# Performance work log

Measured on AMD Instinct MI355X. Metric: run time of the kernel, lower is better.

## Reference

```python
import jax, jax.numpy as jnp
import numpy as np

B = 1024      # batch
DF = 2048     # dim_feat (hard-coded in module)
DIM = 128     # contrastive feature dim
C = 8192      # class_num
P = 8         # pos_size_per_cls
N = 4         # neg_size_per_cls
BN_EPS = 1e-5


def _l2norm(x, axis):
    n = jnp.sqrt(jnp.sum(x * x, axis=axis, keepdims=True))
    return x / jnp.maximum(n, 1e-12)


def setup_inputs() -> dict:
    key = jax.random.key(0)
    ks = jax.random.split(key, 12)
    inp = {
        'mid_feat_q': jax.random.normal(ks[0], (B, DF), jnp.float32),
        'mid_feat_k': jax.random.normal(ks[1], (B, DF), jnp.float32),
        'labels_q': jax.random.randint(ks[2], (B,), 0, C, jnp.int32),
        'labels_k': jax.random.randint(ks[3], (B,), 0, C, jnp.int32),
        'W1': jax.random.normal(ks[4], (DF, DF), jnp.float32) * 0.02,
        'b1': jnp.zeros((DF,), jnp.float32),
        'gamma': jnp.ones((DF,), jnp.float32),
        'beta': jnp.zeros((DF,), jnp.float32),
        'W2': jax.random.normal(ks[5], (DF, DIM), jnp.float32) * 0.02,
        'b2': jnp.zeros((DIM,), jnp.float32),
        'Wlin': jax.random.normal(ks[6], (DF, C), jnp.float32) * 0.02,
        'blin': jnp.zeros((C,), jnp.float32),
        'neg_queue': _l2norm(jax.random.normal(ks[7], (DIM, N * C), jnp.float32), axis=0),
        'pos_queue': _l2norm(jax.random.normal(ks[8], (DIM, P * C), jnp.float32), axis=0),
        'neg_ptr': jnp.zeros((C,), jnp.int32),
        'pos_ptr': jnp.zeros((C,), jnp.int32),
    }
    return inp


def _mlp(x, W1, b1, gamma, beta, W2, b2):
    # Linear -> BatchNorm1d (training: batch stats, biased var) -> ReLU -> Linear
    h = x @ W1 + b1
    mu = jnp.mean(h, axis=0)
    var = jnp.var(h, axis=0)
    h = (h - mu) * jax.lax.rsqrt(var + BN_EPS) * gamma + beta
    h = jax.nn.relu(h)
    return h @ W2 + b2


def reference(mid_feat_q, mid_feat_k, labels_q, labels_k,
              W1, b1, gamma, beta, W2, b2, Wlin, blin,
              neg_queue, pos_queue, neg_ptr, pos_ptr):
    feat_q = _l2norm(_mlp(mid_feat_q, W1, b1, gamma, beta, W2, b2), axis=1)
    feat_k = _l2norm(_mlp(mid_feat_k, W1, b1, gamma, beta, W2, b2), axis=1)

    # per-sample positive block gather: pos_queue[:, l*P:(l+1)*P]
    posq = pos_queue.reshape(DIM, C, P)          # (dim, C, P)
    pg = posq[:, labels_q, :]                    # (dim, B, P)
    pos_list = jnp.einsum('bd,dbp->bp', feat_q, pg)   # (B, P)

    # negatives: full sim then drop each sample's own-class block of N columns
    full_neg = feat_q @ neg_queue                # (B, N*C)
    cols = jnp.arange(N * (C - 1), dtype=jnp.int32)
    idx = cols[None, :] + N * (cols[None, :] >= labels_q[:, None] * N).astype(jnp.int32)
    neg_list = jnp.take_along_axis(full_neg, idx, axis=1)  # (B, N*(C-1))

    sim_batch = feat_q @ feat_k.T                # (B, B)
    labels_batch = (labels_q[:, None] == labels_k[None, :]).astype(jnp.float32)

    sim_con = jnp.concatenate([sim_batch, pos_list, neg_list], axis=1)
    labels_con = jnp.concatenate(
        [labels_batch, jnp.ones_like(pos_list), jnp.zeros_like(neg_list)], axis=1)

    logit_cls_q = mid_feat_q @ Wlin + blin
    logit_cls_k = mid_feat_k @ Wlin + blin

    # sequential dequeue/enqueue over the key batch (world_size=1 all_gather)
    def step(carry, inp):
        nq, nptr, pq, pptr = carry
        kv, c = inp
        npos = nptr[c]
        nq = nq.at[:, c * N + npos].set(kv)
        nptr = nptr.at[c].set((npos + 1) % N)
        ppos = pptr[c]
        pq = pq.at[:, c * P + ppos].set(kv)
        pptr = pptr.at[c].set((ppos + 1) % P)
        return (nq, nptr, pq, pptr), None

    (neg_queue2, neg_ptr2, pos_queue2, pos_ptr2), _ = jax.lax.scan(
        step, (neg_queue, neg_ptr, pos_queue, pos_ptr),
        (jax.lax.stop_gradient(feat_k), labels_k))

    return (sim_con, labels_con, logit_cls_q, logit_cls_k,
            neg_queue2, pos_queue2, neg_ptr2, pos_ptr2)
```

## Files before the change

kernel.cpp:

```cpp
#include <hip/hip_runtime.h>

typedef unsigned short u16;
typedef __bf16 bf16x8 __attribute__((ext_vector_type(8)));
typedef unsigned short ushort8 __attribute__((ext_vector_type(8)));
typedef float f32x4 __attribute__((ext_vector_type(4)));

typedef const __attribute__((address_space(1))) void gv_t;
typedef __attribute__((address_space(3))) void lv_t;

__device__ __forceinline__ u16 f2bf(float f) {
    union { float f; unsigned u; } x; x.f = f;
    unsigned r = x.u + 0x7fffu + ((x.u >> 16) & 1u);
    return (u16)(r >> 16);
}
__device__ __forceinline__ float bf2f(u16 h) {
    union { unsigned u; float f; } x; x.u = ((unsigned)h) << 16; return x.f;
}
__device__ __forceinline__ bf16x8 as_bf(ushort8 u) {
    union { ushort8 u; bf16x8 b; } x; x.u = u; return x.b;
}

__global__ void k_cast(const float* __restrict__ in, u16* __restrict__ out, long nvec) {
    long i = (long)blockIdx.x * blockDim.x + threadIdx.x;
    long stride = (long)gridDim.x * blockDim.x;
    for (; i < nvec; i += stride) {
        float4 v = ((const float4*)in)[i];
        u16 o[4] = {f2bf(v.x), f2bf(v.y), f2bf(v.z), f2bf(v.w)};
        *(unsigned long long*)(out + i * 4) = *(unsigned long long*)o;
    }
}

__global__ void k_castT(const float* __restrict__ in, u16* __restrict__ out,
                        int R, int C) {
    __shared__ u16 tile[32][33];
    int c0 = blockIdx.x * 32, r0 = blockIdx.y * 32;
    int tx = threadIdx.x, ty = threadIdx.y;
#pragma unroll
    for (int i = 0; i < 4; i++)
        tile[ty + 8 * i][tx] = f2bf(in[(size_t)(r0 + ty + 8 * i) * C + c0 + tx]);
    __syncthreads();
#pragma unroll
    for (int i = 0; i < 4; i++)
        out[(size_t)(c0 + ty + 8 * i) * R + r0 + tx] = tile[tx][ty + 8 * i];
}

template <int EPI>
__global__ __launch_bounds__(256, 2) void gemm_bt(
    const u16* A0, const u16* A1, const u16* __restrict__ Bt,
    const float* __restrict__ bias, u16* H0, u16* H1, float* C0, float* C1,
    int lda, int ldb, long long ldc, int n_tiles, int Kchunk,
    const int* __restrict__ labels) {
    __shared__ u16 Al[128 * 32];
    __shared__ u16 Bl[128 * 32];
    const int bx = blockIdx.x;
    const int by = blockIdx.y % n_tiles;
    const int kc = blockIdx.y / n_tiles;
    const int half = blockIdx.z;
    const u16* A = half ? A1 : A0;
    const int m0 = bx * 128, n0 = by * 128;
    const int t = threadIdx.x;
    const int w = t >> 6, l = t & 63;
    const int wm = (w & 1) * 64, wn = (w >> 1) * 64;
    const int quad = l >> 4, ln = l & 15;
    const int srow = t >> 2;
    const int sk = (t & 3) * 8;

    f32x4 acc[4][4];
#pragma unroll
    for (int i = 0; i < 4; i++)
#pragma unroll
        for (int j = 0; j < 4; j++) acc[i][j] = f32x4{};

    u16* lAw = Al + (w << 4) * 32;
    u16* lBw = Bl + (w << 4) * 32;

    const int k_begin = kc * Kchunk;
    for (int k0 = k_begin; k0 < k_begin + Kchunk; k0 += 32) {
        if (k0 != k_begin) __syncthreads();
#pragma unroll
        for (int i = 0; i < 2; i++) {
            __builtin_amdgcn_global_load_lds(
                (gv_t*)(A + (size_t)(m0 + srow + i * 64) * lda + k0 + sk),
                (lv_t*)(lAw + i * 64 * 32), 16, 0, 0);
            __builtin_amdgcn_global_load_lds(
                (gv_t*)(Bt + (size_t)(n0 + srow + i * 64) * ldb + k0 + sk),
                (lv_t*)(lBw + i * 64 * 32), 16, 0, 0);
        }
        __syncthreads();
        bf16x8 af[4], bb[4];
#pragma unroll
        for (int i = 0; i < 4; i++) {
            af[i] = as_bf(*(const ushort8*)(Al + (wm + i * 16 + ln) * 32 + quad * 8));
            bb[i] = as_bf(*(const ushort8*)(Bl + (wn + i * 16 + ln) * 32 + quad * 8));
        }
#pragma unroll
        for (int i = 0; i < 4; i++)
#pragma unroll
            for (int j = 0; j < 4; j++)
                acc[i][j] = __builtin_amdgcn_mfma_f32_16x16x32_bf16(af[i], bb[j], acc[i][j], 0, 0, 0);
    }

    u16* Hs = half ? H1 : H0;
    float* Cs = half ? C1 : C0;
#pragma unroll
    for (int i = 0; i < 4; i++) {
        int row = m0 + wm + i * 16 + quad * 4;
#pragma unroll
        for (int j = 0; j < 4; j++) {
            int col = n0 + wn + j * 16 + ln;
            float bv = 0.f;
            if (EPI == 0 || EPI == 3) { if (bias) bv = bias[col]; }
#pragma unroll
            for (int r = 0; r < 4; r++) {
                int rr = row + r;
                float v = acc[i][j][r] + bv;
                if (EPI == 0) {
                    Cs[(size_t)rr * ldc + col] = v;
                } else if (EPI == 3) {
                    Hs[(size_t)rr * ldc + col] = f2bf(v);
                } else if (EPI == 2) {
                    atomicAdd(Cs + (size_t)rr * ldc + col, v);
                } else {
                    int L4 = labels[rr] * 4;
                    if (col < L4)
                        Cs[(size_t)rr * ldc + 1032 + col] = v;
                    else if (col >= L4 + 4)
                        Cs[(size_t)rr * ldc + 1032 + col - 4] = v;
                }
            }
        }
    }
}

__global__ void k_bn_stats(const u16* __restrict__ Hq, const u16* __restrict__ Hk,
                           float* __restrict__ ps, float* __restrict__ ps2) {
    int half = blockIdx.z;
    const u16* H = half ? Hk : Hq;
    int col = blockIdx.x * 256 + threadIdx.x;
    int r0 = blockIdx.y * 64;
    float s = 0.f, s2 = 0.f;
    for (int r = 0; r < 64; r++) {
        float v = bf2f(H[(size_t)(r0 + r) * 2048 + col]);
        s += v; s2 += v * v;
    }
    size_t o = ((size_t)half * 16 + blockIdx.y) * 2048 + col;
    ps[o] = s; ps2[o] = s2;
}

__global__ void k_bn_final(const float* __restrict__ ps, const float* __restrict__ ps2,
                           const float* __restrict__ gamma, const float* __restrict__ beta,
                           float* __restrict__ scale, float* __restrict__ shift) {
    int idx = blockIdx.x * 256 + threadIdx.x;
    int half = idx >> 11, col = idx & 2047;
    float s = 0.f, s2 = 0.f;
    for (int rb = 0; rb < 16; rb++) {
        size_t o = ((size_t)half * 16 + rb) * 2048 + col;
        s += ps[o]; s2 += ps2[o];
    }
    float mu = s * (1.f / 1024.f);
    float var = s2 * (1.f / 1024.f) - mu * mu;
    float sc = gamma[col] * rsqrtf(var + 1e-5f);
    shift[half * 2048 + col] = beta[col] - mu * sc;
    scale[half * 2048 + col] = sc;
}

__global__ void k_bn_apply(u16* Hq, u16* Hk, const float* __restrict__ scale,
                           const float* __restrict__ shift) {
    int row = blockIdx.x, half = blockIdx.y;
    u16* H = half ? Hk : Hq;
    int col = threadIdx.x * 8;
    ushort8 h = *(ushort8*)(H + (size_t)row * 2048 + col);
    ushort8 o;
#pragma unroll
    for (int k = 0; k < 8; k++) {
        float v = bf2f(h[k]) * scale[half * 2048 + col + k] + shift[half * 2048 + col + k];
        o[k] = f2bf(fmaxf(v, 0.f));
    }
    *(ushort8*)(H + (size_t)row * 2048 + col) = o;
}

__global__ void k_l2norm(const float* __restrict__ Fq, const float* __restrict__ Fk,
                         const float* __restrict__ b2, float* fqf, float* fkf,
                         u16* fqh, u16* fkh) {
    int row = blockIdx.x, half = blockIdx.y, d = threadIdx.x;
    const float* F = half ? Fk : Fq;
    float x = F[(size_t)row * 128 + d] + b2[d];
    float ss = x * x;
#pragma unroll
    for (int off = 32; off >= 1; off >>= 1) ss += __shfl_down(ss, off);
    __shared__ float p[2];
    if ((threadIdx.x & 63) == 0) p[threadIdx.x >> 6] = ss;
    __syncthreads();
    float n = sqrtf(p[0] + p[1]);
    float v = x / fmaxf(n, 1e-12f);
    (half ? fkf : fqf)[(size_t)row * 128 + d] = v;
    (half ? fkh : fqh)[(size_t)row * 128 + d] = f2bf(v);
}

__global__ void k_poslist(const float* __restrict__ fqf, const float* __restrict__ pq,
                          const int* __restrict__ lq, float* out0) {
    int b = blockIdx.x, lane = threadIdx.x;
    int base = lq[b] * 8;
    float acc[8] = {0, 0, 0, 0, 0, 0, 0, 0};
    for (int d = lane; d < 128; d += 64) {
        float f = fqf[(size_t)b * 128 + d];
        const float* pp = pq + (size_t)d * 65536 + base;
        float4 v0 = *(const float4*)pp;
        float4 v1 = *(const float4*)(pp + 4);
        acc[0] += f * v0.x; acc[1] += f * v0.y; acc[2] += f * v0.z; acc[3] += f * v0.w;
        acc[4] += f * v1.x; acc[5] += f * v1.y; acc[6] += f * v1.z; acc[7] += f * v1.w;
    }
#pragma unroll
    for (int off = 32; off >= 1; off >>= 1)
#pragma unroll
        for (int p = 0; p < 8; p++) acc[p] += __shfl_down(acc[p], off);
    if (lane == 0) {
#pragma unroll
        for (int p = 0; p < 8; p++)
            out0[(size_t)b * 33796 + 1024 + p] = acc[p];
    }
}

__global__ void k_labels(const int* __restrict__ lq, const int* __restrict__ lk,
                         float* __restrict__ out1) {
    int b = blockIdx.y;
    int j0 = (blockIdx.x * 256 + threadIdx.x) * 8;
    if (j0 >= 33796) return;
    float* o = out1 + (size_t)b * 33796;
    if (j0 >= 1032 && j0 + 8 <= 33796) {
        float4 z = {0.f, 0.f, 0.f, 0.f};
        *(float4*)(o + j0) = z;
        *(float4*)(o + j0 + 4) = z;
    } else {
        int Lq = lq[b];
        for (int k = 0; k < 8 && j0 + k < 33796; k++) {
            int j = j0 + k;
            o[j] = (j < 1024) ? ((Lq == lk[j]) ? 1.f : 0.f) : (j < 1032 ? 1.f : 0.f);
        }
    }
}

__global__ void k_copyf4(const float* __restrict__ src, float* __restrict__ dst, long nvec) {
    long i = (long)blockIdx.x * blockDim.x + threadIdx.x;
    long stride = (long)gridDim.x * blockDim.x;
    for (; i < nvec; i += stride) ((float4*)dst)[i] = ((const float4*)src)[i];
}

__global__ void k_rank(const int* __restrict__ lk, const int* __restrict__ nptr,
                       const int* __restrict__ pptr, int* __restrict__ counts,
                       int* __restrict__ colN, int* __restrict__ colP) {
    __shared__ int lab[1024];
    int b = threadIdx.x;
    lab[b] = lk[b];
    __syncthreads();
    int c = lab[b];
    int rank = 0, count = 0;
    for (int i = 0; i < 1024; i++) {
        int m = (lab[i] == c);
        count += m;
        rank += (i < b) ? m : 0;
    }
    if (rank == count - 1) counts[c] = count;
    colN[b] = (rank >= count - 4) ? c * 4 + (nptr[c] + rank) % 4 : -1;
    colP[b] = (rank >= count - 8) ? c * 8 + (pptr[c] + rank) % 8 : -1;
}

__global__ void k_scatter(const float* __restrict__ fkf, const int* __restrict__ colN,
                          const int* __restrict__ colP, float* outN, float* outP) {
    int b = blockIdx.x, d = threadIdx.x;
    float v = fkf[(size_t)b * 128 + d];
    int cn = colN[b];
    if (cn >= 0) outN[(size_t)d * 32768 + cn] = v;
    int cp = colP[b];
    if (cp >= 0) outP[(size_t)d * 65536 + cp] = v;
}

__global__ void k_ptrs(const int* __restrict__ nptr, const int* __restrict__ pptr,
                       const int* __restrict__ counts, float* outN, float* outP) {
    int c = blockIdx.x * 256 + threadIdx.x;
    int cnt = counts[c];
    outN[c] = (float)((nptr[c] + cnt) & 3);
    outP[c] = (float)((pptr[c] + cnt) & 7);
}

extern "C" void kernel_launch(void* const* d_in, const int* in_sizes, int n_in,
                              void* d_out, int out_size, void* d_ws, size_t ws_size,
                              hipStream_t stream) {
    const float* midq = (const float*)d_in[0];
    const float* midk = (const float*)d_in[1];
    const int* lq     = (const int*)d_in[2];
    const int* lk     = (const int*)d_in[3];
    const float* W1   = (const float*)d_in[4];
    const float* b1   = (const float*)d_in[5];
    const float* gamma= (const float*)d_in[6];
    const float* beta = (const float*)d_in[7];
    const float* W2   = (const float*)d_in[8];
    const float* b2   = (const float*)d_in[9];
    const float* Wlin = (const float*)d_in[10];
    const float* blin = (const float*)d_in[11];
    const float* nq   = (const float*)d_in[12];
    const float* pq   = (const float*)d_in[13];
    const int* nptr   = (const int*)d_in[14];
    const int* pptr   = (const int*)d_in[15];
    (void)in_sizes; (void)n_in; (void)out_size; (void)ws_size;

    float* out = (float*)d_out;
    const size_t O0 = 0;
    const size_t O1 = 34607104;
    const size_t O2 = 69214208;
    const size_t O3 = 77602816;
    const size_t O4 = 85991424;
    const size_t O5 = 90185728;
    const size_t O6 = 98574336;
    const size_t O7 = 98582528;

    char* ws = (char*)d_ws;
    size_t off = 0;
    auto alloc = [&](size_t bytes) -> char* {
        char* p = ws + off;
        off = (off + bytes + 255) & ~(size_t)255;
        return p;
    };
    u16* W1t   = (u16*)alloc((size_t)2048 * 2048 * 2);
    u16* WlinT = (u16*)alloc((size_t)8192 * 2048 * 2);
    u16* W2t   = (u16*)alloc((size_t)128 * 2048 * 2);
    u16* nqT   = (u16*)alloc((size_t)32768 * 128 * 2);
    u16* midqh = (u16*)alloc((size_t)1024 * 2048 * 2);
    u16* midkh = (u16*)alloc((size_t)1024 * 2048 * 2);
    u16* Hq    = (u16*)alloc((size_t)1024 * 2048 * 2);
    u16* Hk    = (u16*)alloc((size_t)1024 * 2048 * 2);
    float* Fq  = (float*)alloc((size_t)1024 * 128 * 4);
    float* Fk  = (float*)alloc((size_t)1024 * 128 * 4);
    float* fqf = (float*)alloc((size_t)1024 * 128 * 4);
    float* fkf = (float*)alloc((size_t)1024 * 128 * 4);
    u16* fqh   = (u16*)alloc((size_t)1024 * 128 * 2);
    u16* fkh   = (u16*)alloc((size_t)1024 * 128 * 2);
    float* ps  = (float*)alloc((size_t)2 * 16 * 2048 * 4);
    float* ps2 = (float*)alloc((size_t)2 * 16 * 2048 * 4);
    float* scaleA = (float*)alloc((size_t)2 * 2048 * 4);
    float* shiftA = (float*)alloc((size_t)2 * 2048 * 4);
    int* counts = (int*)alloc(8192 * 4);
    int* colN   = (int*)alloc(1024 * 4);
    int* colP   = (int*)alloc(1024 * 4);

    k_cast<<<1024, 256, 0, stream>>>(midq, midqh, (long)1024 * 2048 / 4);
    k_cast<<<1024, 256, 0, stream>>>(midk, midkh, (long)1024 * 2048 / 4);
    dim3 tb(32, 8);
    k_castT<<<dim3(64, 64), tb, 0, stream>>>(W1, W1t, 2048, 2048);
    k_castT<<<dim3(256, 64), tb, 0, stream>>>(Wlin, WlinT, 2048, 8192);
    k_castT<<<dim3(4, 64), tb, 0, stream>>>(W2, W2t, 2048, 128);
    k_castT<<<dim3(1024, 4), tb, 0, stream>>>(nq, nqT, 128, 32768);

    gemm_bt<3><<<dim3(8, 16, 2), 256, 0, stream>>>(midqh, midkh, W1t, b1, Hq, Hk,
        nullptr, nullptr, 2048, 2048, 2048, 16, 2048, nullptr);

    k_bn_stats<<<dim3(8, 16, 2), 256, 0, stream>>>(Hq, Hk, ps, ps2);
    k_bn_final<<<16, 256, 0, stream>>>(ps, ps2, gamma, beta, scaleA, shiftA);
    k_bn_apply<<<dim3(1024, 2), 256, 0, stream>>>(Hq, Hk, scaleA, shiftA);

    hipMemsetAsync(Fq, 0, (size_t)2 * 1024 * 128 * 4, stream);
    hipMemsetAsync(counts, 0, 8192 * 4, stream);

    gemm_bt<2><<<dim3(8, 8, 2), 256, 0, stream>>>(Hq, Hk, W2t, nullptr, nullptr,
        nullptr, Fq, Fk, 2048, 2048, 128, 1, 256, nullptr);

    k_l2norm<<<dim3(1024, 2), 128, 0, stream>>>(Fq, Fk, b2, fqf, fkf, fqh, fkh);

    gemm_bt<0><<<dim3(8, 8, 1), 256, 0, stream>>>(fqh, fqh, fkh, nullptr,
        nullptr, nullptr, out + O0, out + O0, 128, 128, 33796, 8, 128, nullptr);

    k_poslist<<<1024, 64, 0, stream>>>(fqf, pq, lq, out + O0);

    gemm_bt<1><<<dim3(8, 256, 1), 256, 0, stream>>>(fqh, fqh, nqT, nullptr,
        nullptr, nullptr, out + O0, out + O0, 128, 128, 33796, 256, 128, lq);

    k_labels<<<dim3(17, 1024), 256, 0, stream>>>(lq, lk, out + O1);

    gemm_bt<0><<<dim3(8, 64, 2), 256, 0, stream>>>(midqh, midkh, WlinT, blin,
        nullptr, nullptr, out + O2, out + O3, 2048, 2048, 8192, 64, 2048, nullptr);

    k_copyf4<<<2048, 256, 0, stream>>>(nq, out + O4, 4194304 / 4);
    k_copyf4<<<2048, 256, 0, stream>>>(pq, out + O5, 8388608 / 4);

    k_rank<<<1, 1024, 0, stream>>>(lk, nptr, pptr, counts, colN, colP);
    k_scatter<<<1024, 128, 0, stream>>>(fkf, colN, colP, out + O4, out + O5);
    k_ptrs<<<32, 256, 0, stream>>>(nptr, pptr, counts, out + O6, out + O7);
}
```

Baseline: 799.2 us.

## Fuse small kernels, replace split-K atomics with partial buffers, parallelize rank

Merges the two input cast kernels and the two queue copy kernels into single launches. The split-K second-MLP GEMM now writes per-split partial slices instead of using atomicAdd, and the l2norm kernel sums the 8 partials, which also lets the memset go away. The positive-list dot product is folded into the l2norm kernel, and k_rank is spread over 8 blocks instead of one 1024-thread block. The aim is to cut launch count, atomic traffic and serialization, at the cost of a larger partial buffer and extra partial reads.

```diff
diff --git a/kernel.cpp b/kernel.cpp
--- a/kernel.cpp
+++ b/kernel.cpp
@@ -20,7 +20,10 @@
     union { ushort8 u; bf16x8 b; } x; x.u = u; return x.b;
 }
 
-__global__ void k_cast(const float* __restrict__ in, u16* __restrict__ out, long nvec) {
+__global__ void k_cast2(const float* __restrict__ in0, const float* __restrict__ in1,
+                        u16* __restrict__ out0, u16* __restrict__ out1, long nvec) {
+    const float* in = blockIdx.y ? in1 : in0;
+    u16* out = blockIdx.y ? out1 : out0;
     long i = (long)blockIdx.x * blockDim.x + threadIdx.x;
     long stride = (long)gridDim.x * blockDim.x;
     for (; i < nvec; i += stride) {
@@ -119,7 +122,7 @@
                 } else if (EPI == 3) {
                     Hs[(size_t)rr * ldc + col] = f2bf(v);
                 } else if (EPI == 2) {
-                    atomicAdd(Cs + (size_t)rr * ldc + col, v);
+                    Cs[(size_t)kc * (1024 * (size_t)ldc) + (size_t)rr * ldc + col] = v;
                 } else {
                     int L4 = labels[rr] * 4;
                     if (col < L4)
@@ -179,12 +182,16 @@
     *(ushort8*)(H + (size_t)row * 2048 + col) = o;
 }
 
-__global__ void k_l2norm(const float* __restrict__ Fq, const float* __restrict__ Fk,
+__global__ void k_l2norm(const float* __restrict__ Fqp, const float* __restrict__ Fkp,
                          const float* __restrict__ b2, float* fqf, float* fkf,
-                         u16* fqh, u16* fkh) {
+                         u16* fqh, u16* fkh, const float* __restrict__ pq,
+                         const int* __restrict__ lq, float* __restrict__ out0) {
     int row = blockIdx.x, half = blockIdx.y, d = threadIdx.x;
-    const float* F = half ? Fk : Fq;
-    float x = F[(size_t)row * 128 + d] + b2[d];
+    const float* Fp = half ? Fkp : Fqp;
+    float x = b2[d];
+#pragma unroll
+    for (int kc = 0; kc < 8; kc++)
+        x += Fp[(size_t)kc * 131072 + (size_t)row * 128 + d];
     float ss = x * x;
 #pragma unroll
     for (int off = 32; off >= 1; off >>= 1) ss += __shfl_down(ss, off);
@@ -195,29 +202,27 @@
     float v = x / fmaxf(n, 1e-12f);
     (half ? fkf : fqf)[(size_t)row * 128 + d] = v;
     (half ? fkh : fqh)[(size_t)row * 128 + d] = f2bf(v);
-}
-
-__global__ void k_poslist(const float* __restrict__ fqf, const float* __restrict__ pq,
-                          const int* __restrict__ lq, float* out0) {
-    int b = blockIdx.x, lane = threadIdx.x;
-    int base = lq[b] * 8;
-    float acc[8] = {0, 0, 0, 0, 0, 0, 0, 0};
-    for (int d = lane; d < 128; d += 64) {
-        float f = fqf[(size_t)b * 128 + d];
+
+    if (half == 0) {
+        int base = lq[row] * 8;
         const float* pp = pq + (size_t)d * 65536 + base;
         float4 v0 = *(const float4*)pp;
         float4 v1 = *(const float4*)(pp + 4);
-        acc[0] += f * v0.x; acc[1] += f * v0.y; acc[2] += f * v0.z; acc[3] += f * v0.w;
-        acc[4] += f * v1.x; acc[5] += f * v1.y; acc[6] += f * v1.z; acc[7] += f * v1.w;
-    }
-#pragma unroll
-    for (int off = 32; off >= 1; off >>= 1)
-#pragma unroll
-        for (int p = 0; p < 8; p++) acc[p] += __shfl_down(acc[p], off);
-    if (lane == 0) {
-#pragma unroll
-        for (int p = 0; p < 8; p++)
-            out0[(size_t)b * 33796 + 1024 + p] = acc[p];
+        float a[8] = {v * v0.x, v * v0.y, v * v0.z, v * v0.w,
+                      v * v1.x, v * v1.y, v * v1.z, v * v1.w};
+#pragma unroll
+        for (int off = 32; off >= 1; off >>= 1)
+#pragma unroll
+            for (int q = 0; q < 8; q++) a[q] += __shfl_down(a[q], off);
+        __shared__ float pr[2][8];
+        if ((threadIdx.x & 63) == 0) {
+#pragma unroll
+            for (int q = 0; q < 8; q++) pr[threadIdx.x >> 6][q] = a[q];
+        }
+        __syncthreads();
+        if (threadIdx.x < 8)
+            out0[(size_t)row * 33796 + 1024 + threadIdx.x] =
+                pr[0][threadIdx.x] + pr[1][threadIdx.x];
     }
 }
 
@@ -240,19 +245,25 @@
     }
 }
 
-__global__ void k_copyf4(const float* __restrict__ src, float* __restrict__ dst, long nvec) {
+__global__ void k_copy2(const float* __restrict__ s1, float* __restrict__ d1, long n1,
+                        const float* __restrict__ s2, float* __restrict__ d2, long n2) {
     long i = (long)blockIdx.x * blockDim.x + threadIdx.x;
     long stride = (long)gridDim.x * blockDim.x;
-    for (; i < nvec; i += stride) ((float4*)dst)[i] = ((const float4*)src)[i];
+    long tot = n1 + n2;
+    for (; i < tot; i += stride) {
+        if (i < n1) ((float4*)d1)[i] = ((const float4*)s1)[i];
+        else ((float4*)d2)[i - n1] = ((const float4*)s2)[i - n1];
+    }
 }
 
 __global__ void k_rank(const int* __restrict__ lk, const int* __restrict__ nptr,
                        const int* __restrict__ pptr, int* __restrict__ counts,
                        int* __restrict__ colN, int* __restrict__ colP) {
     __shared__ int lab[1024];
-    int b = threadIdx.x;
-    lab[b] = lk[b];
+    int tid = threadIdx.x;
+    for (int i = tid; i < 1024; i += 128) lab[i] = lk[i];
     __syncthreads();
+    int b = blockIdx.x * 128 + tid;
     int c = lab[b];
     int rank = 0, count = 0;
     for (int i = 0; i < 1024; i++) {
@@ -329,8 +340,8 @@
     u16* midkh = (u16*)alloc((size_t)1024 * 2048 * 2);
     u16* Hq    = (u16*)alloc((size_t)1024 * 2048 * 2);
     u16* Hk    = (u16*)alloc((size_t)1024 * 2048 * 2);
-    float* Fq  = (float*)alloc((size_t)1024 * 128 * 4);
-    float* Fk  = (float*)alloc((size_t)1024 * 128 * 4);
+    float* Fq  = (float*)alloc((size_t)8 * 1024 * 128 * 4);
+    float* Fk  = (float*)alloc((size_t)8 * 1024 * 128 * 4);
     float* fqf = (float*)alloc((size_t)1024 * 128 * 4);
     float* fkf = (float*)alloc((size_t)1024 * 128 * 4);
     u16* fqh   = (u16*)alloc((size_t)1024 * 128 * 2);
@@ -343,8 +354,8 @@
     int* colN   = (int*)alloc(1024 * 4);
     int* colP   = (int*)alloc(1024 * 4);
 
-    k_cast<<<1024, 256, 0, stream>>>(midq, midqh, (long)1024 * 2048 / 4);
-    k_cast<<<1024, 256, 0, stream>>>(midk, midkh, (long)1024 * 2048 / 4);
+    k_cast2<<<dim3(1024, 2), 256, 0, stream>>>(midq, midk, midqh, midkh,
+                                               (long)1024 * 2048 / 4);
     dim3 tb(32, 8);
     k_castT<<<dim3(64, 64), tb, 0, stream>>>(W1, W1t, 2048, 2048);
     k_castT<<<dim3(256, 64), tb, 0, stream>>>(Wlin, WlinT, 2048, 8192);
@@ -358,19 +369,17 @@
     k_bn_final<<<16, 256, 0, stream>>>(ps, ps2, gamma, beta, scaleA, shiftA);
     k_bn_apply<<<dim3(1024, 2), 256, 0, stream>>>(Hq, Hk, scaleA, shiftA);
 
-    hipMemsetAsync(Fq, 0, (size_t)2 * 1024 * 128 * 4, stream);
     hipMemsetAsync(counts, 0, 8192 * 4, stream);
 
     gemm_bt<2><<<dim3(8, 8, 2), 256, 0, stream>>>(Hq, Hk, W2t, nullptr, nullptr,
         nullptr, Fq, Fk, 2048, 2048, 128, 1, 256, nullptr);
 
-    k_l2norm<<<dim3(1024, 2), 128, 0, stream>>>(Fq, Fk, b2, fqf, fkf, fqh, fkh);
+    k_l2norm<<<dim3(1024, 2), 128, 0, stream>>>(Fq, Fk, b2, fqf, fkf, fqh, fkh,
+                                                pq, lq, out + O0);
 
     gemm_bt<0><<<dim3(8, 8, 1), 256, 0, stream>>>(fqh, fqh, fkh, nullptr,
         nullptr, nullptr, out + O0, out + O0, 128, 128, 33796, 8, 128, nullptr);
 
-    k_poslist<<<1024, 64, 0, stream>>>(fqf, pq, lq, out + O0);
-
     gemm_bt<1><<<dim3(8, 256, 1), 256, 0, stream>>>(fqh, fqh, nqT, nullptr,
         nullptr, nullptr, out + O0, out + O0, 128, 128, 33796, 256, 128, lq);
 
@@ -379,10 +388,10 @@
     gemm_bt<0><<<dim3(8, 64, 2), 256, 0, stream>>>(midqh, midkh, WlinT, blin,
         nullptr, nullptr, out + O2, out + O3, 2048, 2048, 8192, 64, 2048, nullptr);
 
-    k_copyf4<<<2048, 256, 0, stream>>>(nq, out + O4, 4194304 / 4);
-    k_copyf4<<<2048, 256, 0, stream>>>(pq, out + O5, 8388608 / 4);
-
-    k_rank<<<1, 1024, 0, stream>>>(lk, nptr, pptr, counts, colN, colP);
+    k_copy2<<<2048, 256, 0, stream>>>(nq, out + O4, 4194304 / 4,
+                                      pq, out + O5, 8388608 / 4);
+
+    k_rank<<<8, 128, 0, stream>>>(lk, nptr, pptr, counts, colN, colP);
     k_scatter<<<1024, 128, 0, stream>>>(fkf, colN, colP, out + O4, out + O5);
     k_ptrs<<<32, 256, 0, stream>>>(nptr, pptr, counts, out + O6, out + O7);
 }
```

After: 775.9 us. 1.03x faster.
